# Kernel optimization log

Measured on AMD Instinct MI355X. Metric: run time of the kernel, lower is better.

The kernel has to match this reference:

```python
import jax, jax.numpy as jnp
import numpy as np

TAU_PRE = 2.0
TAU_POST = 2.0
KH, KW = 3, 3
B, CIN, H, W = 16, 64, 66, 66
COUT = 128
HOUT, WOUT = H - KH + 1, W - KW + 1  # stride 1, padding 0


def setup_inputs() -> dict:
    key = jax.random.key(0)
    k1, k2, k3, k4, k5 = jax.random.split(key, 5)
    in_spike = jax.random.uniform(k1, (B, CIN, H, W), dtype=jnp.float32)
    out_spike = jax.random.uniform(k2, (B, COUT, HOUT, WOUT), dtype=jnp.float32)
    trace_pre = jax.random.uniform(k3, (B, CIN, H, W), dtype=jnp.float32)
    trace_post = jax.random.uniform(k4, (B, COUT, HOUT, WOUT), dtype=jnp.float32)
    weight = jax.random.normal(k5, (COUT, CIN, KH, KW), dtype=jnp.float32) * 0.05
    return {"in_spike": in_spike, "out_spike": out_spike,
            "trace_pre": trace_pre, "trace_post": trace_post, "weight": weight}


def reference(in_spike, out_spike, trace_pre, trace_post, weight):
    # Trace decay + spike accumulation (faithful to torch: tr - tr/tau + spike)
    tr_pre = trace_pre - trace_pre / TAU_PRE + in_spike    # [B,Cin,H,W]
    tr_post = trace_post - trace_post / TAU_POST + out_spike  # [B,Cout,Hout,Wout]

    rows = []
    for h in range(KH):
        cols = []
        for w in range(KW):
            pre = in_spike[:, :, h:h + HOUT, w:w + WOUT]   # [B,Cin,Hout,Wout]
            trp = tr_pre[:, :, h:h + HOUT, w:w + WOUT]     # [B,Cin,Hout,Wout]
            wk = weight[:, :, h, w]                        # [Cout,Cin]
            # sum over batch and spatial dims of outer products
            s_pre = jnp.einsum('bopq,bipq->oi', tr_post, pre)      # [Cout,Cin]
            s_post = jnp.einsum('bipq,bopq->oi', trp, out_spike)   # [Cout,Cin]
            cols.append(-wk * s_pre + wk * s_post)
        rows.append(jnp.stack(cols, axis=-1))  # [Cout,Cin,KW]
    delta_w = jnp.stack(rows, axis=-2)          # [Cout,Cin,KH,KW]
    return tr_pre, tr_post, delta_w
```

## Files before the change

### kernel.cpp

```cpp
#include <hip/hip_runtime.h>


typedef unsigned short ushort_t;
typedef unsigned int uint_t;
typedef __attribute__((ext_vector_type(8))) short short8;
typedef __attribute__((ext_vector_type(4))) float floatx4;

#define N_PRE   4460544
#define N_POST  8388608
#define N_DW    73728
#define O_TRPOST 4460544
#define O_DW     12849152
#define BSLICE   4325376

__device__ __forceinline__ ushort_t f2bf(float f) {
  uint_t u = __builtin_bit_cast(uint_t, f);
  u = (u + 0x7FFFu + ((u >> 16) & 1u)) >> 16;
  return (ushort_t)u;
}

__global__ void k_pre(const float* __restrict__ in_sp, const float* __restrict__ tpre,
                      float* __restrict__ o_trpre,
                      ushort_t* __restrict__ B1, ushort_t* __restrict__ B2, int write_ws) {
  int idx = blockIdx.x * 256 + threadIdx.x;
  float tp = tpre[idx], is = in_sp[idx];
  o_trpre[idx] = 0.5f * tp + is;
  if (write_ws) {
    int row = idx / 66;
    int q66 = idx - row * 66;
    ushort_t tpb = f2bf(tp), isb = f2bf(is);
    #pragma unroll
    for (int kw = 0; kw < 3; ++kw) {
      int q = q66 - kw;
      if (q >= 0 && q < 64) {
        B1[kw * BSLICE + row * 64 + q] = tpb;
        B2[kw * BSLICE + row * 64 + q] = isb;
      }
    }
  }
}

__global__ void k_post(const float* __restrict__ out_sp, const float* __restrict__ tpost,
                       float* __restrict__ o_trpost,
                       ushort_t* __restrict__ A1, ushort_t* __restrict__ A2, int write_ws) {
  int idx = blockIdx.x * 256 + threadIdx.x;
  float tp = tpost[idx], os = out_sp[idx];
  o_trpost[idx] = 0.5f * tp + os;
  if (write_ws) {
    A1[idx] = f2bf(os);
    A2[idx] = f2bf(-tp);
  }
}

__global__ __launch_bounds__(256, 2)
void k_mfma(const ushort_t* __restrict__ A1, const ushort_t* __restrict__ A2,
            const ushort_t* __restrict__ B1, const ushort_t* __restrict__ B2,
            float* __restrict__ partials) {
  __shared__ short LA[2][128][72];
  __shared__ short LB[2][64][72];

  const int e = blockIdx.y, kh = e / 3, kw = e - kh * 3;
  const ushort_t* B1e = B1 + kw * BSLICE;
  const ushort_t* B2e = B2 + kw * BSLICE;
  const int t = threadIdx.x, wave = t >> 6, lane = t & 63;
  const int quad = lane >> 4, l16 = lane & 15;

  floatx4 acc[2][4] = {};

  for (int rr = 0; rr < 16; ++rr) {
    const int r = blockIdx.x * 16 + rr;
    const int b = r >> 6, p = r & 63;

    const long baseA = (long)b * 524288 + p * 64;
    #pragma unroll
    for (int it = 0; it < 4; ++it) {
      int c = t + it * 256;
      int o = c >> 3, s = c & 7;
      *(short8*)&LA[0][o][s * 8] = *(const short8*)(A1 + baseA + o * 4096 + s * 8);
      *(short8*)&LA[1][o][s * 8] = *(const short8*)(A2 + baseA + o * 4096 + s * 8);
    }
    const long baseB = (long)b * 270336 + (p + kh) * 64;
    #pragma unroll
    for (int it = 0; it < 2; ++it) {
      int c = t + it * 256;
      int i = c >> 3, s = c & 7;
      *(short8*)&LB[0][i][s * 8] = *(const short8*)(B1e + baseB + i * 4224 + s * 8);
      *(short8*)&LB[1][i][s * 8] = *(const short8*)(B2e + baseB + i * 4224 + s * 8);
    }
    __syncthreads();

    const int ob = wave * 32;
    #pragma unroll
    for (int ks = 0; ks < 2; ++ks) {
      const int col = ks * 32 + quad * 8;
      short8 a00 = *(const short8*)&LA[0][ob + l16][col];
      short8 a01 = *(const short8*)&LA[0][ob + 16 + l16][col];
      short8 a10 = *(const short8*)&LA[1][ob + l16][col];
      short8 a11 = *(const short8*)&LA[1][ob + 16 + l16][col];
      #pragma unroll
      for (int nt = 0; nt < 4; ++nt) {
        short8 b0 = *(const short8*)&LB[0][nt * 16 + l16][col];
        short8 b1 = *(const short8*)&LB[1][nt * 16 + l16][col];
        acc[0][nt] = __builtin_amdgcn_mfma_f32_16x16x32_bf16(a00, b0, acc[0][nt], 0, 0, 0);
        acc[0][nt] = __builtin_amdgcn_mfma_f32_16x16x32_bf16(a10, b1, acc[0][nt], 0, 0, 0);
        acc[1][nt] = __builtin_amdgcn_mfma_f32_16x16x32_bf16(a01, b0, acc[1][nt], 0, 0, 0);
        acc[1][nt] = __builtin_amdgcn_mfma_f32_16x16x32_bf16(a11, b1, acc[1][nt], 0, 0, 0);
      }
    }
    __syncthreads();
  }

  float* slice = partials + ((size_t)(e * 64 + blockIdx.x) * 8192);
  #pragma unroll
  for (int mt = 0; mt < 2; ++mt)
    #pragma unroll
    for (int nt = 0; nt < 4; ++nt)
      #pragma unroll
      for (int rg = 0; rg < 4; ++rg) {
        int o = wave * 32 + mt * 16 + quad * 4 + rg;
        int i = nt * 16 + l16;
        slice[o * 64 + i] = acc[mt][nt][rg];
      }
}

__global__ void k_finalize(const float* __restrict__ partials,
                           const float* __restrict__ weight, float* __restrict__ dw) {
  int tid = blockIdx.x * 256 + threadIdx.x;
  int e = tid >> 13, oi = tid & 8191;
  float s = 0.f;
  #pragma unroll 8
  for (int c = 0; c < 64; ++c) s += partials[(size_t)(e * 64 + c) * 8192 + oi];
  int o = oi >> 6, i = oi & 63;
  int kh = e / 3, kw = e - kh * 3;
  int wi = (o * 64 + i) * 9 + kh * 3 + kw;
  dw[wi] = 0.5f * weight[wi] * s;
}

__global__ void k_naive(const float* __restrict__ out_sp, const float* __restrict__ tpost,
                        const float* __restrict__ tpre, const float* __restrict__ in_sp,
                        const float* __restrict__ weight, float* __restrict__ dw) {
  int tid = blockIdx.x * 256 + threadIdx.x;
  int e = tid >> 13, oi = tid & 8191;
  int o = oi >> 6, i = oi & 63;
  int kh = e / 3, kw = e - kh * 3;
  float acc = 0.f;
  for (int b = 0; b < 16; ++b)
    for (int p = 0; p < 64; ++p) {
      const float* ga = out_sp + ((b * 128 + o) * 64 + p) * 64;
      const float* gn = tpost + ((b * 128 + o) * 64 + p) * 64;
      const float* gb = tpre + ((b * 64 + i) * 66 + p + kh) * 66 + kw;
      const float* gm = in_sp + ((b * 64 + i) * 66 + p + kh) * 66 + kw;
      for (int q = 0; q < 64; ++q) acc += ga[q] * gb[q] - gn[q] * gm[q];
    }
  int wi = (o * 64 + i) * 9 + kh * 3 + kw;
  dw[wi] = 0.5f * weight[wi] * acc;
}

extern "C" void kernel_launch(void* const* d_in, const int* in_sizes, int n_in,
                              void* d_out, int out_size, void* d_ws, size_t ws_size,
                              hipStream_t stream) {
  const float* in_sp  = (const float*)d_in[0];
  const float* out_sp = (const float*)d_in[1];
  const float* tpre   = (const float*)d_in[2];
  const float* tpost  = (const float*)d_in[3];
  const float* weight = (const float*)d_in[4];
  float* out = (float*)d_out;
  float* o_trpre  = out;
  float* o_trpost = out + O_TRPOST;
  float* o_dw     = out + O_DW;

  const size_t WS_NEED = 104333312;
  const int use_mfma = (ws_size >= WS_NEED) ? 1 : 0;
  ushort_t* A1 = (ushort_t*)d_ws;
  ushort_t* A2 = A1 + 8388608;
  ushort_t* B1 = A2 + 8388608;
  ushort_t* B2 = B1 + 3 * BSLICE;
  float* partials = (float*)(B2 + 3 * BSLICE);

  k_pre <<<N_PRE  / 256, 256, 0, stream>>>(in_sp, tpre, o_trpre, B1, B2, use_mfma);
  k_post<<<N_POST / 256, 256, 0, stream>>>(out_sp, tpost, o_trpost, A1, A2, use_mfma);
  if (use_mfma) {
    dim3 g(64, 9);
    k_mfma<<<g, 256, 0, stream>>>(A1, A2, B1, B2, partials);
    k_finalize<<<N_DW / 256, 256, 0, stream>>>(partials, weight, o_dw);
  } else {
    k_naive<<<N_DW / 256, 256, 0, stream>>>(out_sp, tpost, tpre, in_sp, weight, o_dw);
  }
}
```

Baseline: 217.4 us.

## Vectorize elementwise kernels and restructure MFMA kernel with direct LDS loads and swizzle

Vectorizes the trace-update kernels and splits bf16 workspace generation for the pre-synaptic tensor into a row-based kernel with short8 stores. The MFMA kernel now uses 128-thread blocks with output channels split across a new grid dimension. It loads tiles straight into LDS with global_load_lds and uses an XOR swizzle instead of padded rows. The aim is to cut scattered stores, register-staged copies and LDS bank conflicts. In exchange, the pre inputs are read twice and there are more partial-sum slices to reduce.

```diff
diff --git a/kernel.cpp b/kernel.cpp
--- a/kernel.cpp
+++ b/kernel.cpp
@@ -5,6 +5,7 @@
 typedef unsigned int uint_t;
 typedef __attribute__((ext_vector_type(8))) short short8;
 typedef __attribute__((ext_vector_type(4))) float floatx4;
+typedef __attribute__((ext_vector_type(2))) float floatx2;
 
 #define N_PRE   4460544
 #define N_POST  8388608
@@ -13,111 +14,144 @@
 #define O_DW     12849152
 #define BSLICE   4325376
 
+#define GLDS16(g, l) __builtin_amdgcn_global_load_lds( \
+    (const __attribute__((address_space(1))) void*)(g), \
+    (__attribute__((address_space(3))) void*)(l), 16, 0, 0)
+
 __device__ __forceinline__ ushort_t f2bf(float f) {
   uint_t u = __builtin_bit_cast(uint_t, f);
   u = (u + 0x7FFFu + ((u >> 16) & 1u)) >> 16;
   return (ushort_t)u;
 }
 
-__global__ void k_pre(const float* __restrict__ in_sp, const float* __restrict__ tpre,
-                      float* __restrict__ o_trpre,
-                      ushort_t* __restrict__ B1, ushort_t* __restrict__ B2, int write_ws) {
-  int idx = blockIdx.x * 256 + threadIdx.x;
-  float tp = tpre[idx], is = in_sp[idx];
-  o_trpre[idx] = 0.5f * tp + is;
-  if (write_ws) {
-    int row = idx / 66;
-    int q66 = idx - row * 66;
-    ushort_t tpb = f2bf(tp), isb = f2bf(is);
-    #pragma unroll
-    for (int kw = 0; kw < 3; ++kw) {
-      int q = q66 - kw;
-      if (q >= 0 && q < 64) {
-        B1[kw * BSLICE + row * 64 + q] = tpb;
-        B2[kw * BSLICE + row * 64 + q] = isb;
-      }
-    }
+__global__ void k_pre_elem(const float* __restrict__ in_sp, const float* __restrict__ tpre,
+                           float* __restrict__ o_trpre) {
+  int t4 = (blockIdx.x * 256 + threadIdx.x) * 4;
+  floatx4 tp = *(const floatx4*)(tpre + t4);
+  floatx4 is = *(const floatx4*)(in_sp + t4);
+  *(floatx4*)(o_trpre + t4) = 0.5f * tp + is;
+}
+
+__global__ void k_bfill(const float* __restrict__ in_sp, const float* __restrict__ tpre,
+                        ushort_t* __restrict__ B1, ushort_t* __restrict__ B2) {
+  int tid = blockIdx.x * 256 + threadIdx.x;
+  int row = tid >> 3, q8 = (tid & 7) * 8;
+  int g = row * 66 + q8;
+  float ftp[10], fin[10];
+  #pragma unroll
+  for (int k = 0; k < 5; ++k) {
+    floatx2 a = *(const floatx2*)(tpre + g + 2 * k);
+    floatx2 b = *(const floatx2*)(in_sp + g + 2 * k);
+    ftp[2 * k] = a.x; ftp[2 * k + 1] = a.y;
+    fin[2 * k] = b.x; fin[2 * k + 1] = b.y;
+  }
+  ushort_t utp[10], uin[10];
+  #pragma unroll
+  for (int k = 0; k < 10; ++k) { utp[k] = f2bf(ftp[k]); uin[k] = f2bf(fin[k]); }
+  int dst = row * 64 + q8;
+  #pragma unroll
+  for (int kw = 0; kw < 3; ++kw) {
+    short8 v1, v2;
+    #pragma unroll
+    for (int k = 0; k < 8; ++k) { v1[k] = (short)utp[kw + k]; v2[k] = (short)uin[kw + k]; }
+    *(short8*)(B1 + kw * BSLICE + dst) = v1;
+    *(short8*)(B2 + kw * BSLICE + dst) = v2;
   }
 }
 
 __global__ void k_post(const float* __restrict__ out_sp, const float* __restrict__ tpost,
                        float* __restrict__ o_trpost,
                        ushort_t* __restrict__ A1, ushort_t* __restrict__ A2, int write_ws) {
-  int idx = blockIdx.x * 256 + threadIdx.x;
-  float tp = tpost[idx], os = out_sp[idx];
-  o_trpost[idx] = 0.5f * tp + os;
+  int t8 = (blockIdx.x * 256 + threadIdx.x) * 8;
+  floatx4 o0 = *(const floatx4*)(out_sp + t8);
+  floatx4 o1 = *(const floatx4*)(out_sp + t8 + 4);
+  floatx4 p0 = *(const floatx4*)(tpost + t8);
+  floatx4 p1 = *(const floatx4*)(tpost + t8 + 4);
+  *(floatx4*)(o_trpost + t8)     = 0.5f * p0 + o0;
+  *(floatx4*)(o_trpost + t8 + 4) = 0.5f * p1 + o1;
   if (write_ws) {
-    A1[idx] = f2bf(os);
-    A2[idx] = f2bf(-tp);
-  }
-}
-
-__global__ __launch_bounds__(256, 2)
+    short8 va, vn;
+    #pragma unroll
+    for (int k = 0; k < 4; ++k) {
+      va[k] = (short)f2bf(o0[k]); va[k + 4] = (short)f2bf(o1[k]);
+      vn[k] = (short)f2bf(-p0[k]); vn[k + 4] = (short)f2bf(-p1[k]);
+    }
+    *(short8*)(A1 + t8) = va;
+    *(short8*)(A2 + t8) = vn;
+  }
+}
+
+__global__ __launch_bounds__(128, 3)
 void k_mfma(const ushort_t* __restrict__ A1, const ushort_t* __restrict__ A2,
             const ushort_t* __restrict__ B1, const ushort_t* __restrict__ B2,
             float* __restrict__ partials) {
-  __shared__ short LA[2][128][72];
-  __shared__ short LB[2][64][72];
-
-  const int e = blockIdx.y, kh = e / 3, kw = e - kh * 3;
-  const ushort_t* B1e = B1 + kw * BSLICE;
-  const ushort_t* B2e = B2 + kw * BSLICE;
-  const int t = threadIdx.x, wave = t >> 6, lane = t & 63;
-  const int quad = lane >> 4, l16 = lane & 15;
+  __shared__ short LA[8192];
+  __shared__ short LB[8192];
+
+  const int oh = blockIdx.y, e = blockIdx.z;
+  const int kh = e / 3, kw = e - kh * 3;
+  const int t = threadIdx.x, w = t >> 6, l = t & 63;
+  const int quad = l >> 4, l16 = l & 15;
+  const int wo = w * 32;
+
+  const int lrow = l >> 3;
+  const int s_sw = (l & 7) ^ (lrow & 7);
+  const int aoff_lane = lrow * 4096 + s_sw * 8;
+  const int boff_lane = lrow * 4224 + s_sw * 8;
+
+  const ushort_t* PA = (w == 0) ? A1 : A2;
+  const ushort_t* PB = ((w == 0) ? B1 : B2) + kw * BSLICE;
+  short* la = LA + w * 4096;
+  short* lb = LB + w * 4096;
 
   floatx4 acc[2][4] = {};
 
   for (int rr = 0; rr < 16; ++rr) {
     const int r = blockIdx.x * 16 + rr;
     const int b = r >> 6, p = r & 63;
-
-    const long baseA = (long)b * 524288 + p * 64;
-    #pragma unroll
-    for (int it = 0; it < 4; ++it) {
-      int c = t + it * 256;
-      int o = c >> 3, s = c & 7;
-      *(short8*)&LA[0][o][s * 8] = *(const short8*)(A1 + baseA + o * 4096 + s * 8);
-      *(short8*)&LA[1][o][s * 8] = *(const short8*)(A2 + baseA + o * 4096 + s * 8);
-    }
-    const long baseB = (long)b * 270336 + (p + kh) * 64;
-    #pragma unroll
-    for (int it = 0; it < 2; ++it) {
-      int c = t + it * 256;
-      int i = c >> 3, s = c & 7;
-      *(short8*)&LB[0][i][s * 8] = *(const short8*)(B1e + baseB + i * 4224 + s * 8);
-      *(short8*)&LB[1][i][s * 8] = *(const short8*)(B2e + baseB + i * 4224 + s * 8);
-    }
+    const ushort_t* ga = PA + b * 524288 + oh * 262144 + p * 64 + aoff_lane;
+    const ushort_t* gb = PB + b * 270336 + (p + kh) * 64 + boff_lane;
+
     __syncthreads();
-
-    const int ob = wave * 32;
+    #pragma unroll
+    for (int j = 0; j < 8; ++j) {
+      GLDS16(ga + j * 32768, la + j * 512);
+      GLDS16(gb + j * 33792, lb + j * 512);
+    }
+    __syncthreads();
+
     #pragma unroll
     for (int ks = 0; ks < 2; ++ks) {
-      const int col = ks * 32 + quad * 8;
-      short8 a00 = *(const short8*)&LA[0][ob + l16][col];
-      short8 a01 = *(const short8*)&LA[0][ob + 16 + l16][col];
-      short8 a10 = *(const short8*)&LA[1][ob + l16][col];
-      short8 a11 = *(const short8*)&LA[1][ob + 16 + l16][col];
+      const int s0 = ks * 4 + quad;
+      const int o0 = wo + l16, o1 = wo + 16 + l16;
+      const int ca0 = (o0 * 8 + (s0 ^ (o0 & 7))) * 8;
+      const int ca1 = (o1 * 8 + (s0 ^ (o1 & 7))) * 8;
+      short8 a00 = *(const short8*)&LA[ca0];
+      short8 a10 = *(const short8*)&LA[4096 + ca0];
+      short8 a01 = *(const short8*)&LA[ca1];
+      short8 a11 = *(const short8*)&LA[4096 + ca1];
       #pragma unroll
       for (int nt = 0; nt < 4; ++nt) {
-        short8 b0 = *(const short8*)&LB[0][nt * 16 + l16][col];
-        short8 b1 = *(const short8*)&LB[1][nt * 16 + l16][col];
+        const int i = nt * 16 + l16;
+        const int cb = (i * 8 + (s0 ^ (i & 7))) * 8;
+        short8 b0 = *(const short8*)&LB[cb];
+        short8 b1 = *(const short8*)&LB[4096 + cb];
         acc[0][nt] = __builtin_amdgcn_mfma_f32_16x16x32_bf16(a00, b0, acc[0][nt], 0, 0, 0);
         acc[0][nt] = __builtin_amdgcn_mfma_f32_16x16x32_bf16(a10, b1, acc[0][nt], 0, 0, 0);
         acc[1][nt] = __builtin_amdgcn_mfma_f32_16x16x32_bf16(a01, b0, acc[1][nt], 0, 0, 0);
         acc[1][nt] = __builtin_amdgcn_mfma_f32_16x16x32_bf16(a11, b1, acc[1][nt], 0, 0, 0);
       }
     }
-    __syncthreads();
-  }
-
-  float* slice = partials + ((size_t)(e * 64 + blockIdx.x) * 8192);
+  }
+
+  float* slice = partials + (size_t)((e * 64 + blockIdx.x) * 2 + oh) * 4096;
   #pragma unroll
   for (int mt = 0; mt < 2; ++mt)
     #pragma unroll
     for (int nt = 0; nt < 4; ++nt)
       #pragma unroll
       for (int rg = 0; rg < 4; ++rg) {
-        int o = wave * 32 + mt * 16 + quad * 4 + rg;
+        int o = wo + mt * 16 + quad * 4 + rg;
         int i = nt * 16 + l16;
         slice[o * 64 + i] = acc[mt][nt][rg];
       }
@@ -127,12 +161,13 @@
                            const float* __restrict__ weight, float* __restrict__ dw) {
   int tid = blockIdx.x * 256 + threadIdx.x;
   int e = tid >> 13, oi = tid & 8191;
+  int o = oi >> 6, i = oi & 63;
+  int ohh = o >> 6, ol = o & 63;
+  const float* pp = partials + (size_t)e * 524288 + ohh * 4096 + ol * 64 + i;
   float s = 0.f;
   #pragma unroll 8
-  for (int c = 0; c < 64; ++c) s += partials[(size_t)(e * 64 + c) * 8192 + oi];
-  int o = oi >> 6, i = oi & 63;
-  int kh = e / 3, kw = e - kh * 3;
-  int wi = (o * 64 + i) * 9 + kh * 3 + kw;
+  for (int x = 0; x < 64; ++x) s += pp[x * 8192];
+  int wi = (o * 64 + i) * 9 + e;
   dw[wi] = 0.5f * weight[wi] * s;
 }
 
@@ -177,11 +212,12 @@
   ushort_t* B2 = B1 + 3 * BSLICE;
   float* partials = (float*)(B2 + 3 * BSLICE);
 
-  k_pre <<<N_PRE  / 256, 256, 0, stream>>>(in_sp, tpre, o_trpre, B1, B2, use_mfma);
-  k_post<<<N_POST / 256, 256, 0, stream>>>(out_sp, tpost, o_trpost, A1, A2, use_mfma);
+  k_pre_elem<<<N_PRE / 4 / 256, 256, 0, stream>>>(in_sp, tpre, o_trpre);
+  k_post<<<N_POST / 8 / 256, 256, 0, stream>>>(out_sp, tpost, o_trpost, A1, A2, use_mfma);
   if (use_mfma) {
-    dim3 g(64, 9);
-    k_mfma<<<g, 256, 0, stream>>>(A1, A2, B1, B2, partials);
+    k_bfill<<<540672 / 256, 256, 0, stream>>>(in_sp, tpre, B1, B2);
+    dim3 g(64, 2, 9);
+    k_mfma<<<g, 128, 0, stream>>>(A1, A2, B1, B2, partials);
     k_finalize<<<N_DW / 256, 256, 0, stream>>>(partials, weight, o_dw);
   } else {
     k_naive<<<N_DW / 256, 256, 0, stream>>>(out_sp, tpost, tpre, in_sp, weight, o_dw);
```

New measurement: 216.1 us. No clear change (-0.6%).
